# Optimization experiments

Hardware: AMD Instinct MI355X
Metric: run time of the kernel (lower is better)

## Reference

```python
import jax, jax.numpy as jnp
import numpy as np
from itertools import permutations

NODE, BATCH, DIM, STEP = 32, 64, 32, 8
E = NODE * (NODE - 1)          # 992 directed edges (all ordered pairs)
K = 3                          # edge types
MSG_HID = 64; MSG_OUT = 64; N_HID = 64; PRED_LEN = 8


def setup_inputs() -> dict:
    key = jax.random.key(0)
    ks = jax.random.split(key, 12)
    es = jnp.asarray(np.array(list(permutations(range(NODE), 2))).T, dtype=jnp.int32)  # [2, E]
    x = jax.random.normal(ks[0], (BATCH, NODE, DIM, STEP), jnp.float32)
    z = jax.nn.softmax(jax.random.normal(ks[1], (BATCH, E, K), jnp.float32), axis=-1)
    p = lambda k, shape: jax.random.normal(k, shape, jnp.float32) * 0.1
    return dict(
        x=x, z=z, es=es,
        nodes_mask=jnp.zeros((NODE,), jnp.float32),
        edges_mask=jnp.zeros((E,), jnp.float32),
        mask=jnp.zeros((1,), jnp.float32),
        msg_W1=p(ks[2], (K, 2 * DIM, MSG_HID)), msg_b1=jnp.zeros((K, MSG_HID), jnp.float32),
        msg_W2=p(ks[3], (K, MSG_HID, MSG_OUT)), msg_b2=jnp.zeros((K, MSG_OUT), jnp.float32),
        out_W1=p(ks[4], (DIM + MSG_OUT, N_HID)), out_b1=jnp.zeros((N_HID,), jnp.float32),
        out_W2=p(ks[5], (N_HID, N_HID)), out_b2=jnp.zeros((N_HID,), jnp.float32),
        out_W3=p(ks[6], (N_HID, DIM)), out_b3=jnp.zeros((DIM,), jnp.float32),
        ge_Wi=p(ks[7], (3, N_HID, N_HID)), ge_bi=jnp.zeros((3, N_HID), jnp.float32),
        ge_Wh=p(ks[8], (3, N_HID, N_HID)), ge_bh=jnp.zeros((3, N_HID), jnp.float32),
        gn_Wi=p(ks[9], (3, N_HID + DIM, N_HID + DIM)), gn_bi=jnp.zeros((3, N_HID + DIM), jnp.float32),
        gn_Wh=p(ks[10], (3, N_HID + DIM, N_HID + DIM)), gn_bh=jnp.zeros((3, N_HID + DIM), jnp.float32),
    )


def _gru(inp, hid, Wi, bi, Wh, bh):
    # GRUX: state defaults to hidden
    r = jax.nn.sigmoid(inp @ Wi[0] + bi[0] + hid @ Wh[0] + bh[0])
    i = jax.nn.sigmoid(inp @ Wi[1] + bi[1] + hid @ Wh[1] + bh[1])
    n = jnp.tanh(inp @ Wi[2] + bi[2] + r * (hid @ Wh[2] + bh[2]))
    return (1.0 - i) * n + i * hid


def _run(x, z, es, msg_W1, msg_b1, msg_W2, msg_b2,
         out_W1, out_b1, out_W2, out_b2, out_W3, out_b3,
         ge_Wi, ge_bi, ge_Wh, ge_bh, gn_Wi, gn_bi, gn_Wh, gn_bh):
    xp = jnp.transpose(x, (1, 0, 3, 2))   # [node, batch, step, dim]
    zp = jnp.transpose(z, (1, 0, 2))      # [E, batch, K]
    col, row = es[0], es[1]               # 'o2i': col,row = es; aggregate at col
    counts = jnp.clip(jax.ops.segment_sum(jnp.ones((E,), x.dtype), col, num_segments=NODE), 1.0)
    h_node = h_edge = None
    x_m = None
    xs = []
    for t in range(STEP + PRED_LEN):
        x_in = xp[:, :, t, :] if t < STEP else x_m   # [node, batch, dim]
        # edge gather: msg = cat([x[row], x[col]])
        msg = jnp.concatenate([x_in[row], x_in[col]], axis=-1)  # [E, b, 2*dim]
        # per-edge-type 2-layer MLP mixture, weighted by z, normalized by K
        h1 = jax.nn.relu(jnp.einsum('ebi,kih->kebh', msg, msg_W1) + msg_b1[:, None, None, :])
        h2 = jax.nn.relu(jnp.einsum('kebh,kho->kebo', h1, msg_W2) + msg_b2[:, None, None, :])
        msgs = jnp.einsum('kebo,ebk->ebo', h2, zp) / K          # [E, b, msg_out]
        if h_edge is not None:
            msgs = _gru(msgs, h_edge, ge_Wi, ge_bi, ge_Wh, ge_bh)
        # scatter-mean to nodes
        agg = jax.ops.segment_sum(msgs, col, num_segments=NODE) / counts[:, None, None]
        cat = jnp.concatenate([x_in, agg], axis=-1)             # [node, b, dim+msg_out]
        if h_node is not None:
            cat = _gru(cat, h_node, gn_Wi, gn_bi, gn_Wh, gn_bh)
        h = jax.nn.relu(cat @ out_W1 + out_b1)
        h = jax.nn.relu(h @ out_W2 + out_b2)
        delta = h @ out_W3 + out_b3
        x_m = x_in + delta
        h_node, h_edge = cat, msgs
        xs.append(x_m)
    x_hat = jnp.transpose(jnp.stack(xs, axis=2), (1, 0, 3, 2))  # [batch, node, dim, T]
    return x_hat


def reference(x, z, es, nodes_mask, edges_mask, mask,
              msg_W1, msg_b1, msg_W2, msg_b2,
              out_W1, out_b1, out_W2, out_b2, out_W3, out_b3,
              ge_Wi, ge_bi, ge_Wh, ge_bh, gn_Wi, gn_bi, gn_Wh, gn_bh):
    x_hat = _run(x, z, es, msg_W1, msg_b1, msg_W2, msg_b2,
                 out_W1, out_b1, out_W2, out_b2, out_W3, out_b3,
                 ge_Wi, ge_bi, ge_Wh, ge_bh, gn_Wi, gn_bi, gn_Wh, gn_bh)
    return (x_hat[:, :, :, -PRED_LEN:], x_hat, x_hat)
```

## Files before the change

### kernel.cpp

```cpp
#include <hip/hip_runtime.h>
#include <hip/hip_bf16.h>

#define NNODE 32
#define NB    64
#define NDIM  32
#define NSTEP 8
#define NE    992
#define NTT   16

typedef __bf16 bf16;
typedef __attribute__((ext_vector_type(8))) __bf16 bf16x8;
typedef __attribute__((ext_vector_type(4))) __bf16 bf16x4;
typedef __attribute__((ext_vector_type(4))) float  f32x4;

__device__ __forceinline__ f32x4 mfma_bf16(bf16x8 a, bf16x8 b, f32x4 c) {
  return __builtin_amdgcn_mfma_f32_16x16x32_bf16(a, b, c, 0, 0, 0);
}
__device__ __forceinline__ float sigm(float x) { return 1.0f / (1.0f + __expf(-x)); }
__device__ __forceinline__ float tanh_f(float x) {
  x = fminf(fmaxf(x, -15.0f), 15.0f);
  float e = __expf(2.0f * x);
  return (e - 1.0f) / (e + 1.0f);
}

__global__ void prep_weights(
    const float* __restrict__ msgW1, const float* __restrict__ msgW2,
    const float* __restrict__ geWi,  const float* __restrict__ geWh,
    const float* __restrict__ gnWi,  const float* __restrict__ gnWh,
    const float* __restrict__ oW1,   const float* __restrict__ oW2,
    const float* __restrict__ oW3,
    bf16* __restrict__ B1, bf16* __restrict__ B2,
    bf16* __restrict__ GI, bf16* __restrict__ GH,
    bf16* __restrict__ GN,
    bf16* __restrict__ OW1s, bf16* __restrict__ OW2s, bf16* __restrict__ OW3s) {
  int u = blockIdx.x * 256 + threadIdx.x;
  if (u < 12288) {
    int k = u >> 12, i = (u >> 6) & 63, h = u & 63;
    int kf = i >> 5, quad = (i >> 3) & 3, j = i & 7;
    int nn = k * 64 + h, nt = nn >> 4, lane = quad * 16 + (nn & 15);
    int slot = ((nt * 2 + kf) * 64 + lane) * 8 + j;
    B1[slot] = (bf16)msgW1[u];
    GI[slot] = (bf16)geWi[u];
    GH[slot] = (bf16)geWh[u];
    int ntl = h >> 4, lane2 = quad * 16 + (h & 15);
    int slot2 = k * 4096 + ((ntl * 2 + kf) * 64 + lane2) * 8 + j;
    B2[slot2] = (bf16)msgW2[u];
  } else if (u < 39936) {
    int v = u - 12288;
    int kk = v / 9216, rem = v % 9216, i = rem / 96, h = rem % 96;
    int kf = i >> 5, loc = i & 31, quad = loc >> 3, j = loc & 7;
    int nn = kk * 96 + h, nt = nn >> 4, lane = quad * 16 + (nn & 15);
    int slot = ((nt * 3 + kf) * 64 + lane) * 8 + j;
    GN[slot]         = (bf16)gnWi[v];
    GN[27648 + slot] = (bf16)gnWh[v];
  } else if (u < 46080) {
    int v = u - 39936; int i = v >> 6, h = v & 63;
    int kf = i >> 5, loc = i & 31, quad = loc >> 3, j = loc & 7;
    int nt = h >> 4, lane = quad * 16 + (h & 15);
    OW1s[((nt * 3 + kf) * 64 + lane) * 8 + j] = (bf16)oW1[v];
  } else if (u < 50176) {
    int v = u - 46080; int i = v >> 6, h = v & 63;
    int kf = i >> 5, quad = (i >> 3) & 3, j = i & 7;
    int nt = h >> 4, lane = quad * 16 + (h & 15);
    OW2s[((nt * 2 + kf) * 64 + lane) * 8 + j] = (bf16)oW2[v];
  } else if (u < 52224) {
    int v = u - 50176; int i = v >> 5, h = v & 31;
    int kf = i >> 5, quad = (i >> 3) & 3, j = i & 7;
    int nt = h >> 4, lane = quad * 16 + (h & 15);
    OW3s[((nt * 2 + kf) * 64 + lane) * 8 + j] = (bf16)oW3[v];
  }
}

__global__ void copy_x(const float* __restrict__ x, float* __restrict__ xf,
                       bf16* __restrict__ xb) {
  int u = blockIdx.x * 256 + threadIdx.x;
  int n = u >> 11, b = (u >> 5) & 63, d = u & 31;
  float v = x[((b * 32 + n) * 32 + d) * 8 + 0];
  xf[u] = v;
  xb[u] = (bf16)v;
}

__global__ __launch_bounds__(512, 4) void edge_step(
    const bf16* __restrict__ xb, const int* __restrict__ es,
    const float* __restrict__ z,
    const bf16* __restrict__ B1, const bf16* __restrict__ B2,
    const float* __restrict__ mb1, const float* __restrict__ mb2,
    const bf16* __restrict__ GI, const bf16* __restrict__ GH,
    const float* __restrict__ gbi, const float* __restrict__ gbh,
    bf16* __restrict__ hed, int t) {
  __shared__ __align__(16) char scrbuf[51200];
  __shared__ float zL[2][64][3];
  __shared__ float biasL[768];
  bf16 (*A)[64][72]   = (bf16(*)[64][72])scrbuf;
  bf16 (*A2)[64][200] = (bf16(*)[64][200])scrbuf;

  int e0 = blockIdx.x * 2, tid = threadIdx.x;
  int c0_ = es[e0],     r0 = es[NE + e0];
  int c1_ = es[e0 + 1], r1 = es[NE + e0 + 1];
  for (int u = tid; u < 768; u += 512)
    biasL[u] = (u < 192) ? mb1[u] : (u < 384) ? mb2[u - 192]
             : (u < 576) ? gbi[u - 384] : gbh[u - 576];
  for (int u = tid; u < 384; u += 512) {
    int pe = u / 192, rem = u % 192, b = rem / 3, k = rem % 3;
    zL[pe][b][k] = z[(b * NE + e0 + pe) * 3 + k];
  }
  for (int u = tid; u < 1024; u += 512) {
    int pe = u >> 9, c = u & 511;
    int b = c >> 3, i8 = c & 7;
    int nrow = pe ? r1 : r0, ncol = pe ? c1_ : c0_;
    const bf16* src = (i8 < 4) ? (xb + nrow * 2048 + b * 32 + i8 * 8)
                               : (xb + ncol * 2048 + b * 32 + (i8 - 4) * 8);
    *(bf16x8*)&A[pe][b][i8 * 8] = *(const bf16x8*)src;
  }
  __syncthreads();
  int wv = tid >> 6, ln = tid & 63, quad = ln >> 4, l16 = ln & 15;
  int rg = wv & 3, cg = wv >> 2;
  int m = rg * 16 + l16;
  bf16x8 af[2][2];
#pragma unroll
  for (int pe = 0; pe < 2; pe++)
#pragma unroll
    for (int kf = 0; kf < 2; kf++)
      af[pe][kf] = *(const bf16x8*)&A[pe][m][kf * 32 + quad * 8];
  __syncthreads();
  f32x4 acc1[2][6];
#pragma unroll
  for (int pe = 0; pe < 2; pe++)
#pragma unroll
    for (int q = 0; q < 6; q++) { f32x4 zz = {0.f,0.f,0.f,0.f}; acc1[pe][q] = zz; }
#pragma unroll
  for (int j = 0; j < 6; j++) {
    int nt = cg * 6 + j;
    bf16x8 w0 = *(const bf16x8*)&B1[(nt * 2 + 0) * 512 + ln * 8];
    bf16x8 w1 = *(const bf16x8*)&B1[(nt * 2 + 1) * 512 + ln * 8];
#pragma unroll
    for (int pe = 0; pe < 2; pe++) {
      acc1[pe][j] = mfma_bf16(af[pe][0], w0, acc1[pe][j]);
      acc1[pe][j] = mfma_bf16(af[pe][1], w1, acc1[pe][j]);
    }
  }
#pragma unroll
  for (int j = 0; j < 6; j++) {
    int nt = cg * 6 + j;
    int n = nt * 16 + l16;
    float bias = biasL[n];
#pragma unroll
    for (int pe = 0; pe < 2; pe++)
#pragma unroll
      for (int r = 0; r < 4; r++) {
        float v = acc1[pe][j][r] + bias;
        A2[pe][rg * 16 + quad * 4 + r][n] = (bf16)(v > 0.f ? v : 0.f);
      }
  }
  __syncthreads();
  f32x4 acc2[2][3][2];
#pragma unroll
  for (int pe = 0; pe < 2; pe++)
#pragma unroll
    for (int kt = 0; kt < 3; kt++)
#pragma unroll
      for (int oi = 0; oi < 2; oi++) { f32x4 zz = {0.f,0.f,0.f,0.f}; acc2[pe][kt][oi] = zz; }
#pragma unroll
  for (int kt = 0; kt < 3; kt++) {
    bf16x8 a2f[2][2];
#pragma unroll
    for (int pe = 0; pe < 2; pe++)
#pragma unroll
      for (int kf = 0; kf < 2; kf++)
        a2f[pe][kf] = *(const bf16x8*)&A2[pe][m][kt * 64 + kf * 32 + quad * 8];
#pragma unroll
    for (int oi = 0; oi < 2; oi++) {
      int ot = cg * 2 + oi;
      bf16x8 w0 = *(const bf16x8*)&B2[kt * 4096 + (ot * 2 + 0) * 512 + ln * 8];
      bf16x8 w1 = *(const bf16x8*)&B2[kt * 4096 + (ot * 2 + 1) * 512 + ln * 8];
#pragma unroll
      for (int pe = 0; pe < 2; pe++) {
        acc2[pe][kt][oi] = mfma_bf16(a2f[pe][0], w0, acc2[pe][kt][oi]);
        acc2[pe][kt][oi] = mfma_bf16(a2f[pe][1], w1, acc2[pe][kt][oi]);
      }
    }
  }
  __syncthreads();
#pragma unroll
  for (int pe = 0; pe < 2; pe++)
#pragma unroll
    for (int r = 0; r < 4; r++) {
      int b = rg * 16 + quad * 4 + r;
      float z0 = zL[pe][b][0], z1 = zL[pe][b][1], z2 = zL[pe][b][2];
#pragma unroll
      for (int oi = 0; oi < 2; oi++) {
        int o = (cg * 2 + oi) * 16 + l16;
        float h0 = acc2[pe][0][oi][r] + biasL[192 + o];       h0 = h0 > 0.f ? h0 : 0.f;
        float h1 = acc2[pe][1][oi][r] + biasL[192 + 64 + o];  h1 = h1 > 0.f ? h1 : 0.f;
        float h2 = acc2[pe][2][oi][r] + biasL[192 + 128 + o]; h2 = h2 > 0.f ? h2 : 0.f;
        A[pe][b][o] = (bf16)((h0 * z0 + h1 * z1 + h2 * z2) * (1.0f / 3.0f));
      }
    }
  if (t > 0) {
    __syncthreads();
    bf16x8 ai[2][2], ah[2][2];
#pragma unroll
    for (int pe = 0; pe < 2; pe++) {
      const bf16* hrow = hed + (e0 + pe) * 4096 + m * 64;
#pragma unroll
      for (int kf = 0; kf < 2; kf++) {
        ai[pe][kf] = *(const bf16x8*)&A[pe][m][kf * 32 + quad * 8];
        ah[pe][kf] = *(const bf16x8*)(hrow + kf * 32 + quad * 8);
      }
    }
#pragma unroll
    for (int oi = 0; oi < 2; oi++) {
      int ot = cg * 2 + oi;
      f32x4 gr[2], gi2[2], gni2[2], gnh2[2];
#pragma unroll
      for (int pe = 0; pe < 2; pe++) {
        f32x4 zz = {0.f,0.f,0.f,0.f};
        gr[pe] = zz; gi2[pe] = zz; gni2[pe] = zz; gnh2[pe] = zz;
      }
#pragma unroll
      for (int g = 0; g < 2; g++) {
        int nt = g * 4 + ot;
        bf16x8 wi0 = *(const bf16x8*)&GI[(nt * 2 + 0) * 512 + ln * 8];
        bf16x8 wi1 = *(const bf16x8*)&GI[(nt * 2 + 1) * 512 + ln * 8];
        bf16x8 wh0 = *(const bf16x8*)&GH[(nt * 2 + 0) * 512 + ln * 8];
        bf16x8 wh1 = *(const bf16x8*)&GH[(nt * 2 + 1) * 512 + ln * 8];
#pragma unroll
        for (int pe = 0; pe < 2; pe++) {
          f32x4 a = g ? gi2[pe] : gr[pe];
          a = mfma_bf16(ai[pe][0], wi0, a);
          a = mfma_bf16(ai[pe][1], wi1, a);
          a = mfma_bf16(ah[pe][0], wh0, a);
          a = mfma_bf16(ah[pe][1], wh1, a);
          if (g) gi2[pe] = a; else gr[pe] = a;
        }
      }
      {
        int nt = 8 + ot;
        bf16x8 wi0 = *(const bf16x8*)&GI[(nt * 2 + 0) * 512 + ln * 8];
        bf16x8 wi1 = *(const bf16x8*)&GI[(nt * 2 + 1) * 512 + ln * 8];
        bf16x8 wh0 = *(const bf16x8*)&GH[(nt * 2 + 0) * 512 + ln * 8];
        bf16x8 wh1 = *(const bf16x8*)&GH[(nt * 2 + 1) * 512 + ln * 8];
#pragma unroll
        for (int pe = 0; pe < 2; pe++) {
          gni2[pe] = mfma_bf16(ai[pe][0], wi0, gni2[pe]);
          gni2[pe] = mfma_bf16(ai[pe][1], wi1, gni2[pe]);
          gnh2[pe] = mfma_bf16(ah[pe][0], wh0, gnh2[pe]);
          gnh2[pe] = mfma_bf16(ah[pe][1], wh1, gnh2[pe]);
        }
      }
#pragma unroll
      for (int pe = 0; pe < 2; pe++)
#pragma unroll
        for (int r = 0; r < 4; r++) {
          int b = rg * 16 + quad * 4 + r;
          int o = ot * 16 + l16;
          float xr = gr[pe][r]   + biasL[384 + o]       + biasL[576 + o];
          float xi = gi2[pe][r]  + biasL[384 + 64 + o]  + biasL[576 + 64 + o];
          float xn = gni2[pe][r] + biasL[384 + 128 + o];
          float hn = gnh2[pe][r] + biasL[576 + 128 + o];
          float rgt = sigm(xr);
          float ig  = sigm(xi);
          float ng  = tanh_f(xn + rgt * hn);
          float hv  = (float)hed[(e0 + pe) * 4096 + b * 64 + o];
          A[pe][b][o] = (bf16)((1.0f - ig) * ng + ig * hv);
        }
    }
  }
  __syncthreads();
  for (int u = tid; u < 1024; u += 512) {
    int pe = u >> 9, c = u & 511;
    int b = c >> 3, j = c & 7;
    *(bf16x8*)(hed + (e0 + pe) * 4096 + b * 64 + j * 8) = *(const bf16x8*)&A[pe][b][j * 8];
  }
}

__global__ __launch_bounds__(256) void node_kernel(
    const float* __restrict__ x, const bf16* __restrict__ hed,
    float* __restrict__ xf, bf16* __restrict__ xb, float* __restrict__ hnode,
    const bf16* __restrict__ GN,
    const float* __restrict__ gnbi, const float* __restrict__ gnbh,
    const bf16* __restrict__ OW1, const float* __restrict__ ob1,
    const bf16* __restrict__ OW2, const float* __restrict__ ob2,
    const bf16* __restrict__ OW3, const float* __restrict__ ob3,
    float* __restrict__ out, int t) {
  __shared__ float aggf[16][64];
  __shared__ float xinf[16][32];
  __shared__ float hvf[16][96];
  __shared__ __align__(16) bf16 c0b[16][112];
  __shared__ __align__(16) bf16 hvb[16][112];
  __shared__ float gsum[2][16][290];
  __shared__ __align__(16) bf16 cnb[16][112];
  __shared__ __align__(16) bf16 s1b[16][112];
  __shared__ __align__(16) bf16 s2b[16][112];
  int nq = blockIdx.x, n = nq >> 2, q = nq & 3;
  int tid = threadIdx.x;
  {
    int r = tid >> 4, o4 = tid & 15;
    const bf16x4* bp = (const bf16x4*)hed + (size_t)n * 31 * 1024 + (q * 16 + r) * 16 + o4;
    float sx = 0.f, sy = 0.f, sz = 0.f, sw = 0.f;
#pragma unroll
    for (int e2 = 0; e2 < 31; e2++) {
      bf16x4 v = bp[e2 * 1024];
      sx += (float)v[0]; sy += (float)v[1]; sz += (float)v[2]; sw += (float)v[3];
    }
    const float inv = 1.0f / 31.0f;
    sx *= inv; sy *= inv; sz *= inv; sw *= inv;
    int o = o4 * 4;
    aggf[r][o] = sx; aggf[r][o + 1] = sy; aggf[r][o + 2] = sz; aggf[r][o + 3] = sw;
    c0b[r][32 + o] = (bf16)sx; c0b[r][33 + o] = (bf16)sy;
    c0b[r][34 + o] = (bf16)sz; c0b[r][35 + o] = (bf16)sw;
  }
  if (tid < 128) {
    int r = tid >> 3, d0 = (tid & 7) * 4;
    int b = q * 16 + r;
#pragma unroll
    for (int k = 0; k < 4; k++) {
      float v = xf[n * 2048 + b * 32 + d0 + k];
      xinf[r][d0 + k] = v;
      c0b[r][d0 + k] = (bf16)v;
    }
  }
  if (t > 0) {
    int r = tid >> 4, cb = (tid & 15) * 6;
    int row = n * 64 + q * 16 + r;
#pragma unroll
    for (int k = 0; k < 6; k++) {
      float v = hnode[row * 96 + cb + k];
      hvf[r][cb + k] = v;
      hvb[r][cb + k] = (bf16)v;
    }
  }
  __syncthreads();
  int wv = tid >> 6, ln = tid & 63, quad = ln >> 4, l16 = ln & 15;
  if (t > 0) {
    int mat = wv >> 1, sel = wv & 1;
    const bf16(*Ab)[112] = mat ? hvb : c0b;
    bf16x8 af[3];
#pragma unroll
    for (int kf = 0; kf < 3; kf++)
      af[kf] = *(const bf16x8*)&Ab[l16][kf * 32 + quad * 8];
    const bf16* W = GN + mat * 27648;
    f32x4 accn[9];
#pragma unroll
    for (int q2 = 0; q2 < 9; q2++) { f32x4 zz = {0.f,0.f,0.f,0.f}; accn[q2] = zz; }
#pragma unroll
    for (int nt2 = 0; nt2 < 9; nt2++) {
      int nt = sel * 9 + nt2;
#pragma unroll
      for (int kf = 0; kf < 3; kf++) {
        bf16x8 bfrag = *(const bf16x8*)&W[((nt * 3 + kf) * 64 + ln) * 8];
        accn[nt2] = mfma_bf16(af[kf], bfrag, accn[nt2]);
      }
    }
#pragma unroll
    for (int nt2 = 0; nt2 < 9; nt2++) {
      int col = (sel * 9 + nt2) * 16 + l16;
#pragma unroll
      for (int rr = 0; rr < 4; rr++)
        gsum[mat][quad * 4 + rr][col] = accn[nt2][rr];
    }
  }
  __syncthreads();
  {
    int r = tid >> 4, cb = (tid & 15) * 6;
    int row = n * 64 + q * 16 + r;
#pragma unroll
    for (int k = 0; k < 6; k++) {
      int c = cb + k;
      float v;
      if (t > 0) {
        float xr = gsum[0][r][c] + gnbi[c] + gsum[1][r][c] + gnbh[c];
        float xi = gsum[0][r][96 + c] + gnbi[96 + c] + gsum[1][r][96 + c] + gnbh[96 + c];
        float xn = gsum[0][r][192 + c] + gnbi[192 + c];
        float hn = gsum[1][r][192 + c] + gnbh[192 + c];
        float rg = sigm(xr);
        float ig = sigm(xi);
        float ng = tanh_f(xn + rg * hn);
        v = (1.0f - ig) * ng + ig * hvf[r][c];
      } else {
        v = (c < 32) ? xinf[r][c] : aggf[r][c - 32];
      }
      cnb[r][c] = (bf16)v;
      hnode[row * 96 + c] = v;
    }
  }
  __syncthreads();
  {
    bf16x8 af[3];
#pragma unroll
    for (int kf = 0; kf < 3; kf++)
      af[kf] = *(const bf16x8*)&cnb[l16][kf * 32 + quad * 8];
    f32x4 accn = {0.f, 0.f, 0.f, 0.f};
#pragma unroll
    for (int kf = 0; kf < 3; kf++) {
      bf16x8 bfrag = *(const bf16x8*)&OW1[((wv * 3 + kf) * 64 + ln) * 8];
      accn = mfma_bf16(af[kf], bfrag, accn);
    }
    int col = wv * 16 + l16;
    float bias = ob1[col];
#pragma unroll
    for (int rr = 0; rr < 4; rr++) {
      float vv = accn[rr] + bias;
      s1b[quad * 4 + rr][col] = (bf16)(vv > 0.f ? vv : 0.f);
    }
  }
  __syncthreads();
  {
    bf16x8 af[2];
#pragma unroll
    for (int kf = 0; kf < 2; kf++)
      af[kf] = *(const bf16x8*)&s1b[l16][kf * 32 + quad * 8];
    f32x4 accn = {0.f, 0.f, 0.f, 0.f};
#pragma unroll
    for (int kf = 0; kf < 2; kf++) {
      bf16x8 bfrag = *(const bf16x8*)&OW2[((wv * 2 + kf) * 64 + ln) * 8];
      accn = mfma_bf16(af[kf], bfrag, accn);
    }
    int col = wv * 16 + l16;
    float bias = ob2[col];
#pragma unroll
    for (int rr = 0; rr < 4; rr++) {
      float vv = accn[rr] + bias;
      s2b[quad * 4 + rr][col] = (bf16)(vv > 0.f ? vv : 0.f);
    }
  }
  __syncthreads();
  if (wv < 2) {
    bf16x8 af[2];
#pragma unroll
    for (int kf = 0; kf < 2; kf++)
      af[kf] = *(const bf16x8*)&s2b[l16][kf * 32 + quad * 8];
    f32x4 accn = {0.f, 0.f, 0.f, 0.f};
#pragma unroll
    for (int kf = 0; kf < 2; kf++) {
      bf16x8 bfrag = *(const bf16x8*)&OW3[((wv * 2 + kf) * 64 + ln) * 8];
      accn = mfma_bf16(af[kf], bfrag, accn);
    }
    int d = wv * 16 + l16;
    float bias = ob3[d];
#pragma unroll
    for (int rr = 0; rr < 4; rr++) {
      int r = quad * 4 + rr;
      int b = q * 16 + r;
      float xm = xinf[r][d] + accn[rr] + bias;
      int base = (b * 32 + n) * 32 + d;
      out[524288 + base * 16 + t] = xm;
      out[1572864 + base * 16 + t] = xm;
      if (t >= NSTEP) out[base * 8 + (t - NSTEP)] = xm;
      float vnext = (t + 1 < NSTEP) ? x[base * 8 + (t + 1)] : xm;
      xf[n * 2048 + b * 32 + d] = vnext;
      xb[n * 2048 + b * 32 + d] = (bf16)vnext;
    }
  }
}

extern "C" void kernel_launch(void* const* d_in, const int* in_sizes, int n_in,
                              void* d_out, int out_size, void* d_ws, size_t ws_size,
                              hipStream_t stream) {
  const float* x     = (const float*)d_in[0];
  const float* z     = (const float*)d_in[1];
  const int*   es    = (const int*)d_in[2];
  const float* msgW1 = (const float*)d_in[6];
  const float* msgb1 = (const float*)d_in[7];
  const float* msgW2 = (const float*)d_in[8];
  const float* msgb2 = (const float*)d_in[9];
  const float* oW1   = (const float*)d_in[10];
  const float* ob1   = (const float*)d_in[11];
  const float* oW2   = (const float*)d_in[12];
  const float* ob2   = (const float*)d_in[13];
  const float* oW3   = (const float*)d_in[14];
  const float* ob3   = (const float*)d_in[15];
  const float* geWi  = (const float*)d_in[16];
  const float* gebi  = (const float*)d_in[17];
  const float* geWh  = (const float*)d_in[18];
  const float* gebh  = (const float*)d_in[19];
  const float* gnWi  = (const float*)d_in[20];
  const float* gnbi  = (const float*)d_in[21];
  const float* gnWh  = (const float*)d_in[22];
  const float* gnbh  = (const float*)d_in[23];
  float* out = (float*)d_out;

  char* p = (char*)d_ws;
  bf16*  hed   = (bf16*)p;   p += (size_t)NE * 4096 * 2;
  float* xf    = (float*)p;  p += 65536 * 4;
  bf16*  xb    = (bf16*)p;   p += 65536 * 2;
  float* hnode = (float*)p;  p += 196608 * 4;
  bf16*  B1sw  = (bf16*)p;   p += 12288 * 2;
  bf16*  B2sw  = (bf16*)p;   p += 12288 * 2;
  bf16*  GIsw  = (bf16*)p;   p += 12288 * 2;
  bf16*  GHsw  = (bf16*)p;   p += 12288 * 2;
  bf16*  GNsw  = (bf16*)p;   p += 55296 * 2;
  bf16*  OW1s  = (bf16*)p;   p += 6144 * 2;
  bf16*  OW2s  = (bf16*)p;   p += 4096 * 2;
  bf16*  OW3s  = (bf16*)p;   p += 2048 * 2;

  prep_weights<<<204, 256, 0, stream>>>(msgW1, msgW2, geWi, geWh, gnWi, gnWh,
                                        oW1, oW2, oW3,
                                        B1sw, B2sw, GIsw, GHsw, GNsw,
                                        OW1s, OW2s, OW3s);
  copy_x<<<256, 256, 0, stream>>>(x, xf, xb);

  for (int t = 0; t < NTT; t++) {
    edge_step<<<NE / 2, 512, 0, stream>>>(xb, es, z, B1sw, B2sw, msgb1, msgb2,
                                          GIsw, GHsw, gebi, gebh, hed, t);
    node_kernel<<<128, 256, 0, stream>>>(x, hed, xf, xb, hnode, GNsw, gnbi, gnbh,
                                         OW1s, ob1, OW2s, ob2, OW3s, ob3,
                                         out, t);
  }
}
```

Before: 614.2 us.

## Factor first message layer into per-node projections precomputed in node kernel

The first edge-MLP layer applied to the concatenation [x_row, x_col] is split into two per-node projections P = x·W1_top + b1 and Q = x·W1_bottom. These are computed once per node, in an init kernel and then at the end of each node_kernel step, and stored in a PQ buffer. The edge kernel then only gathers P[row] + Q[col] and applies ReLU, dropping the per-edge first-layer MFMAs and one barrier. In exchange, each edge reads a larger 384-wide bf16 gather per batch row instead of 64 bf16 of x, and the sum is rounded to bf16 before the add.

```diff
diff --git a/kernel.cpp b/kernel.cpp
--- a/kernel.cpp
+++ b/kernel.cpp
@@ -80,79 +80,68 @@
   xb[u] = (bf16)v;
 }
 
+__global__ __launch_bounds__(256) void pq_init(
+    const bf16* __restrict__ xb, const bf16* __restrict__ B1,
+    const float* __restrict__ mb1, bf16* __restrict__ PQ) {
+  int n = blockIdx.x, tid = threadIdx.x;
+  int wv = tid >> 6, ln = tid & 63, quad = ln >> 4, l16 = ln & 15;
+  bf16x8 xfrag = *(const bf16x8*)(xb + n * 2048 + (wv * 16 + l16) * 32 + quad * 8);
+  bf16* pqbase = PQ + ((size_t)(n * 64 + wv * 16)) * 384;
+#pragma unroll
+  for (int c2 = 0; c2 < 24; c2++) {
+    int nt = c2 >> 1, kf = c2 & 1;
+    bf16x8 bfrag = *(const bf16x8*)&B1[(nt * 2 + kf) * 512 + ln * 8];
+    f32x4 acc = {0.f, 0.f, 0.f, 0.f};
+    acc = mfma_bf16(xfrag, bfrag, acc);
+    int col = nt * 16 + l16;
+    float badd = kf ? 0.f : mb1[col];
+#pragma unroll
+    for (int rr = 0; rr < 4; rr++)
+      pqbase[(quad * 4 + rr) * 384 + kf * 192 + col] = (bf16)(acc[rr] + badd);
+  }
+}
+
 __global__ __launch_bounds__(512, 4) void edge_step(
-    const bf16* __restrict__ xb, const int* __restrict__ es,
+    const bf16* __restrict__ PQ, const int* __restrict__ es,
     const float* __restrict__ z,
-    const bf16* __restrict__ B1, const bf16* __restrict__ B2,
-    const float* __restrict__ mb1, const float* __restrict__ mb2,
+    const bf16* __restrict__ B2,
+    const float* __restrict__ mb2,
     const bf16* __restrict__ GI, const bf16* __restrict__ GH,
     const float* __restrict__ gbi, const float* __restrict__ gbh,
     bf16* __restrict__ hed, int t) {
   __shared__ __align__(16) char scrbuf[51200];
   __shared__ float zL[2][64][3];
-  __shared__ float biasL[768];
+  __shared__ float biasL[576];
   bf16 (*A)[64][72]   = (bf16(*)[64][72])scrbuf;
   bf16 (*A2)[64][200] = (bf16(*)[64][200])scrbuf;
 
   int e0 = blockIdx.x * 2, tid = threadIdx.x;
   int c0_ = es[e0],     r0 = es[NE + e0];
   int c1_ = es[e0 + 1], r1 = es[NE + e0 + 1];
-  for (int u = tid; u < 768; u += 512)
-    biasL[u] = (u < 192) ? mb1[u] : (u < 384) ? mb2[u - 192]
-             : (u < 576) ? gbi[u - 384] : gbh[u - 576];
+  for (int u = tid; u < 576; u += 512)
+    biasL[u] = (u < 192) ? mb2[u] : (u < 384) ? gbi[u - 192] : gbh[u - 384];
   for (int u = tid; u < 384; u += 512) {
     int pe = u / 192, rem = u % 192, b = rem / 3, k = rem % 3;
     zL[pe][b][k] = z[(b * NE + e0 + pe) * 3 + k];
   }
-  for (int u = tid; u < 1024; u += 512) {
-    int pe = u >> 9, c = u & 511;
-    int b = c >> 3, i8 = c & 7;
+  for (int u = tid; u < 3072; u += 512) {
+    int pe = u / 1536, rem = u - pe * 1536;
+    int b = rem / 24, c8 = rem - b * 24;
     int nrow = pe ? r1 : r0, ncol = pe ? c1_ : c0_;
-    const bf16* src = (i8 < 4) ? (xb + nrow * 2048 + b * 32 + i8 * 8)
-                               : (xb + ncol * 2048 + b * 32 + (i8 - 4) * 8);
-    *(bf16x8*)&A[pe][b][i8 * 8] = *(const bf16x8*)src;
+    bf16x8 pv = *(const bf16x8*)&PQ[((size_t)(nrow * 64 + b)) * 384 + c8 * 8];
+    bf16x8 qv = *(const bf16x8*)&PQ[((size_t)(ncol * 64 + b)) * 384 + 192 + c8 * 8];
+    bf16x8 hv;
+#pragma unroll
+    for (int j2 = 0; j2 < 8; j2++) {
+      float s = (float)pv[j2] + (float)qv[j2];
+      hv[j2] = (bf16)(s > 0.f ? s : 0.f);
+    }
+    *(bf16x8*)&A2[pe][b][c8 * 8] = hv;
   }
   __syncthreads();
   int wv = tid >> 6, ln = tid & 63, quad = ln >> 4, l16 = ln & 15;
   int rg = wv & 3, cg = wv >> 2;
   int m = rg * 16 + l16;
-  bf16x8 af[2][2];
-#pragma unroll
-  for (int pe = 0; pe < 2; pe++)
-#pragma unroll
-    for (int kf = 0; kf < 2; kf++)
-      af[pe][kf] = *(const bf16x8*)&A[pe][m][kf * 32 + quad * 8];
-  __syncthreads();
-  f32x4 acc1[2][6];
-#pragma unroll
-  for (int pe = 0; pe < 2; pe++)
-#pragma unroll
-    for (int q = 0; q < 6; q++) { f32x4 zz = {0.f,0.f,0.f,0.f}; acc1[pe][q] = zz; }
-#pragma unroll
-  for (int j = 0; j < 6; j++) {
-    int nt = cg * 6 + j;
-    bf16x8 w0 = *(const bf16x8*)&B1[(nt * 2 + 0) * 512 + ln * 8];
-    bf16x8 w1 = *(const bf16x8*)&B1[(nt * 2 + 1) * 512 + ln * 8];
-#pragma unroll
-    for (int pe = 0; pe < 2; pe++) {
-      acc1[pe][j] = mfma_bf16(af[pe][0], w0, acc1[pe][j]);
-      acc1[pe][j] = mfma_bf16(af[pe][1], w1, acc1[pe][j]);
-    }
-  }
-#pragma unroll
-  for (int j = 0; j < 6; j++) {
-    int nt = cg * 6 + j;
-    int n = nt * 16 + l16;
-    float bias = biasL[n];
-#pragma unroll
-    for (int pe = 0; pe < 2; pe++)
-#pragma unroll
-      for (int r = 0; r < 4; r++) {
-        float v = acc1[pe][j][r] + bias;
-        A2[pe][rg * 16 + quad * 4 + r][n] = (bf16)(v > 0.f ? v : 0.f);
-      }
-  }
-  __syncthreads();
   f32x4 acc2[2][3][2];
 #pragma unroll
   for (int pe = 0; pe < 2; pe++)
@@ -190,9 +179,9 @@
 #pragma unroll
       for (int oi = 0; oi < 2; oi++) {
         int o = (cg * 2 + oi) * 16 + l16;
-        float h0 = acc2[pe][0][oi][r] + biasL[192 + o];       h0 = h0 > 0.f ? h0 : 0.f;
-        float h1 = acc2[pe][1][oi][r] + biasL[192 + 64 + o];  h1 = h1 > 0.f ? h1 : 0.f;
-        float h2 = acc2[pe][2][oi][r] + biasL[192 + 128 + o]; h2 = h2 > 0.f ? h2 : 0.f;
+        float h0 = acc2[pe][0][oi][r] + biasL[o];       h0 = h0 > 0.f ? h0 : 0.f;
+        float h1 = acc2[pe][1][oi][r] + biasL[64 + o];  h1 = h1 > 0.f ? h1 : 0.f;
+        float h2 = acc2[pe][2][oi][r] + biasL[128 + o]; h2 = h2 > 0.f ? h2 : 0.f;
         A[pe][b][o] = (bf16)((h0 * z0 + h1 * z1 + h2 * z2) * (1.0f / 3.0f));
       }
     }
@@ -254,10 +243,10 @@
         for (int r = 0; r < 4; r++) {
           int b = rg * 16 + quad * 4 + r;
           int o = ot * 16 + l16;
-          float xr = gr[pe][r]   + biasL[384 + o]       + biasL[576 + o];
-          float xi = gi2[pe][r]  + biasL[384 + 64 + o]  + biasL[576 + 64 + o];
-          float xn = gni2[pe][r] + biasL[384 + 128 + o];
-          float hn = gnh2[pe][r] + biasL[576 + 128 + o];
+          float xr = gr[pe][r]   + biasL[192 + o]       + biasL[384 + o];
+          float xi = gi2[pe][r]  + biasL[256 + o]       + biasL[448 + o];
+          float xn = gni2[pe][r] + biasL[320 + o];
+          float hn = gnh2[pe][r] + biasL[512 + o];
           float rgt = sigm(xr);
           float ig  = sigm(xi);
           float ng  = tanh_f(xn + rgt * hn);
@@ -276,12 +265,14 @@
 
 __global__ __launch_bounds__(256) void node_kernel(
     const float* __restrict__ x, const bf16* __restrict__ hed,
-    float* __restrict__ xf, bf16* __restrict__ xb, float* __restrict__ hnode,
+    float* __restrict__ xf, float* __restrict__ hnode,
     const bf16* __restrict__ GN,
     const float* __restrict__ gnbi, const float* __restrict__ gnbh,
     const bf16* __restrict__ OW1, const float* __restrict__ ob1,
     const bf16* __restrict__ OW2, const float* __restrict__ ob2,
     const bf16* __restrict__ OW3, const float* __restrict__ ob3,
+    const bf16* __restrict__ B1, const float* __restrict__ mb1,
+    bf16* __restrict__ PQ,
     float* __restrict__ out, int t) {
   __shared__ float aggf[16][64];
   __shared__ float xinf[16][32];
@@ -292,6 +283,7 @@
   __shared__ __align__(16) bf16 cnb[16][112];
   __shared__ __align__(16) bf16 s1b[16][112];
   __shared__ __align__(16) bf16 s2b[16][112];
+  __shared__ __align__(16) bf16 xnb[16][40];
   int nq = blockIdx.x, n = nq >> 2, q = nq & 3;
   int tid = threadIdx.x;
   {
@@ -386,15 +378,15 @@
   }
   __syncthreads();
   {
-    bf16x8 af[3];
+    bf16x8 af3[3];
 #pragma unroll
     for (int kf = 0; kf < 3; kf++)
-      af[kf] = *(const bf16x8*)&cnb[l16][kf * 32 + quad * 8];
+      af3[kf] = *(const bf16x8*)&cnb[l16][kf * 32 + quad * 8];
     f32x4 accn = {0.f, 0.f, 0.f, 0.f};
 #pragma unroll
     for (int kf = 0; kf < 3; kf++) {
       bf16x8 bfrag = *(const bf16x8*)&OW1[((wv * 3 + kf) * 64 + ln) * 8];
-      accn = mfma_bf16(af[kf], bfrag, accn);
+      accn = mfma_bf16(af3[kf], bfrag, accn);
     }
     int col = wv * 16 + l16;
     float bias = ob1[col];
@@ -406,15 +398,15 @@
   }
   __syncthreads();
   {
-    bf16x8 af[2];
+    bf16x8 af2[2];
 #pragma unroll
     for (int kf = 0; kf < 2; kf++)
-      af[kf] = *(const bf16x8*)&s1b[l16][kf * 32 + quad * 8];
+      af2[kf] = *(const bf16x8*)&s1b[l16][kf * 32 + quad * 8];
     f32x4 accn = {0.f, 0.f, 0.f, 0.f};
 #pragma unroll
     for (int kf = 0; kf < 2; kf++) {
       bf16x8 bfrag = *(const bf16x8*)&OW2[((wv * 2 + kf) * 64 + ln) * 8];
-      accn = mfma_bf16(af[kf], bfrag, accn);
+      accn = mfma_bf16(af2[kf], bfrag, accn);
     }
     int col = wv * 16 + l16;
     float bias = ob2[col];
@@ -426,15 +418,15 @@
   }
   __syncthreads();
   if (wv < 2) {
-    bf16x8 af[2];
+    bf16x8 af2[2];
 #pragma unroll
     for (int kf = 0; kf < 2; kf++)
-      af[kf] = *(const bf16x8*)&s2b[l16][kf * 32 + quad * 8];
+      af2[kf] = *(const bf16x8*)&s2b[l16][kf * 32 + quad * 8];
     f32x4 accn = {0.f, 0.f, 0.f, 0.f};
 #pragma unroll
     for (int kf = 0; kf < 2; kf++) {
       bf16x8 bfrag = *(const bf16x8*)&OW3[((wv * 2 + kf) * 64 + ln) * 8];
-      accn = mfma_bf16(af[kf], bfrag, accn);
+      accn = mfma_bf16(af2[kf], bfrag, accn);
     }
     int d = wv * 16 + l16;
     float bias = ob3[d];
@@ -449,7 +441,24 @@
       if (t >= NSTEP) out[base * 8 + (t - NSTEP)] = xm;
       float vnext = (t + 1 < NSTEP) ? x[base * 8 + (t + 1)] : xm;
       xf[n * 2048 + b * 32 + d] = vnext;
-      xb[n * 2048 + b * 32 + d] = (bf16)vnext;
+      xnb[r][d] = (bf16)vnext;
+    }
+  }
+  __syncthreads();
+  {
+    bf16x8 xfrag = *(const bf16x8*)&xnb[l16][quad * 8];
+    bf16* pqbase = PQ + ((size_t)(n * 64 + q * 16)) * 384;
+#pragma unroll
+    for (int i2 = 0; i2 < 6; i2++) {
+      int c2 = wv * 6 + i2, nt = c2 >> 1, kf = c2 & 1;
+      bf16x8 bfrag = *(const bf16x8*)&B1[(nt * 2 + kf) * 512 + ln * 8];
+      f32x4 acc = {0.f, 0.f, 0.f, 0.f};
+      acc = mfma_bf16(xfrag, bfrag, acc);
+      int col = nt * 16 + l16;
+      float badd = kf ? 0.f : mb1[col];
+#pragma unroll
+      for (int rr = 0; rr < 4; rr++)
+        pqbase[(quad * 4 + rr) * 384 + kf * 192 + col] = (bf16)(acc[rr] + badd);
     }
   }
 }
@@ -485,6 +494,7 @@
   float* xf    = (float*)p;  p += 65536 * 4;
   bf16*  xb    = (bf16*)p;   p += 65536 * 2;
   float* hnode = (float*)p;  p += 196608 * 4;
+  bf16*  PQ    = (bf16*)p;   p += (size_t)32 * 64 * 384 * 2;
   bf16*  B1sw  = (bf16*)p;   p += 12288 * 2;
   bf16*  B2sw  = (bf16*)p;   p += 12288 * 2;
   bf16*  GIsw  = (bf16*)p;   p += 12288 * 2;
@@ -499,12 +509,13 @@
                                         B1sw, B2sw, GIsw, GHsw, GNsw,
                                         OW1s, OW2s, OW3s);
   copy_x<<<256, 256, 0, stream>>>(x, xf, xb);
+  pq_init<<<32, 256, 0, stream>>>(xb, B1sw, msgb1, PQ);
 
   for (int t = 0; t < NTT; t++) {
-    edge_step<<<NE / 2, 512, 0, stream>>>(xb, es, z, B1sw, B2sw, msgb1, msgb2,
+    edge_step<<<NE / 2, 512, 0, stream>>>(PQ, es, z, B2sw, msgb2,
                                           GIsw, GHsw, gebi, gebh, hed, t);
-    node_kernel<<<128, 256, 0, stream>>>(x, hed, xf, xb, hnode, GNsw, gnbi, gnbh,
+    node_kernel<<<128, 256, 0, stream>>>(x, hed, xf, hnode, GNsw, gnbi, gnbh,
                                          OW1s, ob1, OW2s, ob2, OW3s, ob3,
-                                         out, t);
-  }
-}
+                                         B1sw, msgb1, PQ, out, t);
+  }
+}
```

After: 653.2 us. 6.4% more time.
